# Kernel optimization log

Measured on AMD Instinct MI355X. Metric: run time of the kernel, lower is better.

## Reference

```python
import jax, jax.numpy as jnp
import numpy as np

N_HEAD = 16
LN_EPS = 1e-5


def setup_inputs() -> dict:
    key = jax.random.key(0)
    ks = jax.random.split(key, 12)
    B, S, D = 4, 1024, 1024
    s = 1.0 / np.sqrt(D)
    return {
        "Q": jax.random.normal(ks[0], (B, S, D), jnp.float32),
        "K": jax.random.normal(ks[1], (B, S, D), jnp.float32),
        "V": jax.random.normal(ks[2], (B, S, D), jnp.float32),
        # Linear weights stored torch-style [out, in]
        "Wq": jax.random.normal(ks[3], (D, D), jnp.float32) * s,
        "bq": jnp.zeros((D,), jnp.float32),
        "Wk": jax.random.normal(ks[4], (D, D), jnp.float32) * s,
        "bk": jnp.zeros((D,), jnp.float32),
        "Wv": jax.random.normal(ks[5], (D, D), jnp.float32) * s,
        "bv": jnp.zeros((D,), jnp.float32),
        "Wo": jax.random.normal(ks[6], (D, D), jnp.float32) * s,
        "bo": jnp.zeros((D,), jnp.float32),
        "ln_g": jnp.ones((D,), jnp.float32),
        "ln_b": jnp.zeros((D,), jnp.float32),
    }


def _layer_norm(x, g, b):
    mu = jnp.mean(x, axis=-1, keepdims=True)
    var = jnp.mean(jnp.square(x - mu), axis=-1, keepdims=True)
    return (x - mu) * jax.lax.rsqrt(var + LN_EPS) * g + b


def reference(Q, K, V, Wq, bq, Wk, bk, Wv, bv, Wo, bo, ln_g, ln_b):
    B, S, D = Q.shape
    H = N_HEAD
    dk = D // H
    # projections, split heads: [B, H, S, dk]
    q = (Q @ Wq.T + bq).reshape(B, S, H, dk).transpose(0, 2, 1, 3)
    k = (K @ Wk.T + bk).reshape(B, S, H, dk).transpose(0, 2, 1, 3)
    v = (V @ Wv.T + bv).reshape(B, S, H, dk).transpose(0, 2, 1, 3)
    scores = jnp.einsum("bhqd,bhkd->bhqk", q, k) / np.sqrt(dk)
    # NOTE: original module applies softmax twice (F.softmax then nn.Softmax)
    attn = jax.nn.softmax(jax.nn.softmax(scores, axis=-1), axis=-1)
    ctx = jnp.einsum("bhqk,bhkd->bhqd", attn, v)  # [B, H, S, dk]
    ctx = ctx.transpose(0, 2, 1, 3).reshape(B, S, D)
    out = ctx @ Wo.T + bo
    return _layer_norm(out + Q, ln_g, ln_b)
```

## Files before the change

kernel.cpp:

```cpp
#include <hip/hip_runtime.h>
#include <cstdint>
#include <cstddef>


typedef unsigned short ushort_t;
typedef __attribute__((ext_vector_type(8))) short bf16x8;
typedef __attribute__((ext_vector_type(8))) unsigned short us8;
typedef __attribute__((ext_vector_type(4))) unsigned short us4;
typedef __attribute__((ext_vector_type(4))) float f32x4;

#define MFMA16(a, b, c) __builtin_amdgcn_mfma_f32_16x16x32_bf16((a), (b), (c), 0, 0, 0)

__device__ __forceinline__ float b2f(ushort_t u) {
  union { unsigned int i; float f; } x; x.i = ((unsigned int)u) << 16; return x.f;
}
__device__ __forceinline__ ushort_t f2b(float f) {
  union { unsigned int i; float f; } x; x.f = f;
  unsigned int r = (x.i + 0x7FFFu + ((x.i >> 16) & 1u)) >> 16;
  return (ushort_t)r;
}
__device__ __forceinline__ us8 cvt8(float4 a, float4 b) {
  us8 r;
  r[0] = f2b(a.x); r[1] = f2b(a.y); r[2] = f2b(a.z); r[3] = f2b(a.w);
  r[4] = f2b(b.x); r[5] = f2b(b.y); r[6] = f2b(b.z); r[7] = f2b(b.w);
  return r;
}

__global__ __launch_bounds__(256, 8) void cvt4_kernel(
    const float* __restrict__ w0, const float* __restrict__ w1,
    const float* __restrict__ w2, const float* __restrict__ w3,
    ushort_t* __restrict__ dst) {
  const int which = blockIdx.y;
  const float* src = (which == 0) ? w0 : (which == 1) ? w1 : (which == 2) ? w2 : w3;
  const int i = (blockIdx.x * 256 + threadIdx.x) * 8;
  const float4 a = *(const float4*)(src + i);
  const float4 b = *(const float4*)(src + i + 4);
  *(us8*)(dst + (size_t)which * 1048576 + i) = cvt8(a, b);
}

__global__ __launch_bounds__(256, 6) void qkv_proj_kernel(
    const float* __restrict__ Qin, const float* __restrict__ Kin,
    const float* __restrict__ Vin,
    const ushort_t* __restrict__ wq, const ushort_t* __restrict__ wk,
    const ushort_t* __restrict__ wv,
    const float* __restrict__ bq, const float* __restrict__ bk,
    const float* __restrict__ bv,
    ushort_t* __restrict__ qb, ushort_t* __restrict__ kb,
    ushort_t* __restrict__ vb) {
  __shared__ __align__(16) ushort_t Asl[64 * 32];
  __shared__ __align__(16) ushort_t Bsl[128 * 32];
  const float* A; const ushort_t* W; const float* bias; float scale;
  if (blockIdx.z == 0)      { A = Qin; W = wq; bias = bq; scale = 0.125f; }
  else if (blockIdx.z == 1) { A = Kin; W = wk; bias = bk; scale = 1.0f; }
  else                      { A = Vin; W = wv; bias = bv; scale = 1.0f; }
  const int l = blockIdx.x;
  const int xcd = l & 7, ii = l >> 3;
  const int m0 = (xcd * 8 + (ii >> 3)) * 64;
  const int n0 = (ii & 7) * 128;
  const int tid = threadIdx.x;
  const int wave = tid >> 6, lane = tid & 63;
  const int l15 = lane & 15, quad = lane >> 4;
  const int wn = wave * 32;

  const int ra = tid >> 2, ca = (tid & 3) * 8;
  const int rb1 = (tid + 256) >> 2;

  const float* Ap = A + (size_t)(m0 + ra) * 1024 + ca;
  const ushort_t* Bp0 = W + (size_t)(n0 + ra) * 1024 + ca;
  const ushort_t* Bp1 = W + (size_t)(n0 + rb1) * 1024 + ca;

  float4 al = *(const float4*)(Ap), ah = *(const float4*)(Ap + 4);
  us8 rb0v = *(const us8*)(Bp0);
  us8 rb1v = *(const us8*)(Bp1);

  f32x4 acc[4][2] = {};
  for (int k0 = 0; k0 < 1024; k0 += 32) {
    __syncthreads();
    *(us8*)(Asl + ra * 32 + ca) = cvt8(al, ah);
    *(us8*)(Bsl + ra * 32 + ca) = rb0v;
    *(us8*)(Bsl + rb1 * 32 + ca) = rb1v;
    __syncthreads();
    if (k0 + 32 < 1024) {
      const int k = k0 + 32;
      al = *(const float4*)(Ap + k); ah = *(const float4*)(Ap + k + 4);
      rb0v = *(const us8*)(Bp0 + k);
      rb1v = *(const us8*)(Bp1 + k);
    }
    bf16x8 af[4], bfr[2];
#pragma unroll
    for (int s = 0; s < 4; ++s)
      af[s] = *(const bf16x8*)(Asl + (s * 16 + l15) * 32 + quad * 8);
#pragma unroll
    for (int s = 0; s < 2; ++s)
      bfr[s] = *(const bf16x8*)(Bsl + (wn + s * 16 + l15) * 32 + quad * 8);
#pragma unroll
    for (int ms = 0; ms < 4; ++ms)
#pragma unroll
      for (int ns = 0; ns < 2; ++ns)
        acc[ms][ns] = MFMA16(af[ms], bfr[ns], acc[ms][ns]);
  }

  if (blockIdx.z != 2) {
    ushort_t* outp = (blockIdx.z == 0) ? qb : kb;
#pragma unroll
    for (int ns = 0; ns < 2; ++ns) {
      const int col = n0 + wn + ns * 16 + l15;
      const float bv_ = bias[col];
#pragma unroll
      for (int ms = 0; ms < 4; ++ms) {
        const int rowb = m0 + ms * 16 + quad * 4;
#pragma unroll
        for (int r = 0; r < 4; ++r) {
          outp[(size_t)(rowb + r) * 1024 + col] =
              f2b((acc[ms][ns][r] + bv_) * scale);
        }
      }
    }
  } else {
#pragma unroll
    for (int ns = 0; ns < 2; ++ns) {
      const int col = n0 + wn + ns * 16 + l15;
      const float bv_ = bias[col];
      const int h = col >> 6, d = col & 63;
#pragma unroll
      for (int ms = 0; ms < 4; ++ms) {
        const int i0 = m0 + ms * 16 + quad * 4;
        const int b = i0 >> 10, s0 = i0 & 1023;
        us4 pack;
#pragma unroll
        for (int r = 0; r < 4; ++r) pack[r] = f2b(acc[ms][ns][r] + bv_);
        *(us4*)(vb + ((size_t)(b * 16 + h) * 64 + d) * 1024 + s0) = pack;
      }
    }
  }
}

__global__ __launch_bounds__(256, 4) void attn_kernel(
    const ushort_t* __restrict__ qb, const ushort_t* __restrict__ kb,
    const ushort_t* __restrict__ vb, ushort_t* __restrict__ ctx) {
  __shared__ __align__(16) ushort_t Qs[64 * 72];
  __shared__ __align__(16) ushort_t Ks[64 * 72];
  __shared__ __align__(16) ushort_t Vt[64 * 72];
  __shared__ __align__(16) ushort_t Ps[4][16 * 68];

  const int tid = threadIdx.x, wave = tid >> 6, lane = tid & 63;
  const int l15 = lane & 15, quad = lane >> 4;
  const int l = blockIdx.x;
  const int xcd = l & 7, ii = l >> 3;
  const int bh = xcd * 8 + (ii >> 4);
  const int q0 = (ii & 15) * 64;
  const int b = bh >> 4, h = bh & 15;
  const ushort_t* qg = qb + ((size_t)b << 20) + h * 64;
  const ushort_t* kg = kb + ((size_t)b << 20) + h * 64;
  const ushort_t* vg = vb + ((size_t)bh << 16);

  const int kr0 = tid >> 3, kc0 = (tid & 7) * 8;
  const int kr1 = (tid + 256) >> 3, kc1 = kc0;

  *(us8*)(Qs + kr0 * 72 + kc0) = *(const us8*)(qg + (size_t)(q0 + kr0) * 1024 + kc0);
  *(us8*)(Qs + kr1 * 72 + kc1) = *(const us8*)(qg + (size_t)(q0 + kr1) * 1024 + kc1);

  float z1[4] = {0.f, 0.f, 0.f, 0.f};
  us8 rk0 = *(const us8*)(kg + (size_t)kr0 * 1024 + kc0);
  us8 rk1 = *(const us8*)(kg + (size_t)kr1 * 1024 + kc1);
  for (int kt = 0; kt < 16; ++kt) {
    __syncthreads();
    *(us8*)(Ks + kr0 * 72 + kc0) = rk0;
    *(us8*)(Ks + kr1 * 72 + kc1) = rk1;
    __syncthreads();
    if (kt < 15) {
      rk0 = *(const us8*)(kg + (size_t)((kt + 1) * 64 + kr0) * 1024 + kc0);
      rk1 = *(const us8*)(kg + (size_t)((kt + 1) * 64 + kr1) * 1024 + kc1);
    }
    f32x4 sc[4] = {};
#pragma unroll
    for (int kk = 0; kk < 2; ++kk) {
      const bf16x8 aq = *(const bf16x8*)(Qs + (wave * 16 + l15) * 72 + kk * 32 + quad * 8);
#pragma unroll
      for (int ns = 0; ns < 4; ++ns) {
        const bf16x8 bk_ = *(const bf16x8*)(Ks + (ns * 16 + l15) * 72 + kk * 32 + quad * 8);
        sc[ns] = MFMA16(aq, bk_, sc[ns]);
      }
    }
#pragma unroll
    for (int ns = 0; ns < 4; ++ns)
#pragma unroll
      for (int r = 0; r < 4; ++r) z1[r] += __expf(sc[ns][r]);
  }
  float iz1[4];
#pragma unroll
  for (int r = 0; r < 4; ++r) {
    float s = z1[r];
#pragma unroll
    for (int off = 1; off < 16; off <<= 1) s += __shfl_xor(s, off, 64);
    iz1[r] = 1.0f / s;
  }

  f32x4 oac[4] = {};
  float z2[4] = {0.f, 0.f, 0.f, 0.f};
  rk0 = *(const us8*)(kg + (size_t)kr0 * 1024 + kc0);
  rk1 = *(const us8*)(kg + (size_t)kr1 * 1024 + kc1);
  us8 rv0 = *(const us8*)(vg + (size_t)kr0 * 1024 + kc0);
  us8 rv1 = *(const us8*)(vg + (size_t)kr1 * 1024 + kc1);
  for (int kt = 0; kt < 16; ++kt) {
    __syncthreads();
    *(us8*)(Ks + kr0 * 72 + kc0) = rk0;
    *(us8*)(Ks + kr1 * 72 + kc1) = rk1;
    *(us8*)(Vt + kr0 * 72 + kc0) = rv0;
    *(us8*)(Vt + kr1 * 72 + kc1) = rv1;
    __syncthreads();
    if (kt < 15) {
      rk0 = *(const us8*)(kg + (size_t)((kt + 1) * 64 + kr0) * 1024 + kc0);
      rk1 = *(const us8*)(kg + (size_t)((kt + 1) * 64 + kr1) * 1024 + kc1);
      rv0 = *(const us8*)(vg + (size_t)kr0 * 1024 + (kt + 1) * 64 + kc0);
      rv1 = *(const us8*)(vg + (size_t)kr1 * 1024 + (kt + 1) * 64 + kc1);
    }
    f32x4 sc[4] = {};
#pragma unroll
    for (int kk = 0; kk < 2; ++kk) {
      const bf16x8 aq = *(const bf16x8*)(Qs + (wave * 16 + l15) * 72 + kk * 32 + quad * 8);
#pragma unroll
      for (int ns = 0; ns < 4; ++ns) {
        const bf16x8 bk_ = *(const bf16x8*)(Ks + (ns * 16 + l15) * 72 + kk * 32 + quad * 8);
        sc[ns] = MFMA16(aq, bk_, sc[ns]);
      }
    }
#pragma unroll
    for (int ns = 0; ns < 4; ++ns)
#pragma unroll
      for (int r = 0; r < 4; ++r) {
        const float p1 = __expf(sc[ns][r]) * iz1[r];
        const float e2 = __expf(p1);
        z2[r] += e2;
        Ps[wave][(quad * 4 + r) * 68 + ns * 16 + l15] = f2b(e2);
      }
    __asm__ __volatile__("s_waitcnt lgkmcnt(0)" ::: "memory");
#pragma unroll
    for (int kk = 0; kk < 2; ++kk) {
      const ushort_t* pp = &Ps[wave][l15 * 68 + kk * 32 + quad * 8];
      union { us4 hseg[2]; bf16x8 v; } u;
      u.hseg[0] = *(const us4*)pp;
      u.hseg[1] = *(const us4*)(pp + 4);
      const bf16x8 ap = u.v;
#pragma unroll
      for (int ns2 = 0; ns2 < 4; ++ns2) {
        const bf16x8 bv_ = *(const bf16x8*)(Vt + (ns2 * 16 + l15) * 72 + kk * 32 + quad * 8);
        oac[ns2] = MFMA16(ap, bv_, oac[ns2]);
      }
    }
  }

#pragma unroll
  for (int r = 0; r < 4; ++r) {
    float s = z2[r];
#pragma unroll
    for (int off = 1; off < 16; off <<= 1) s += __shfl_xor(s, off, 64);
    z2[r] = s;
  }
#pragma unroll
  for (int ns2 = 0; ns2 < 4; ++ns2) {
    const int d = ns2 * 16 + l15;
#pragma unroll
    for (int r = 0; r < 4; ++r) {
      const int s = q0 + wave * 16 + quad * 4 + r;
      ctx[((size_t)(b * 1024 + s)) * 1024 + h * 64 + d] = f2b(oac[ns2][r] / z2[r]);
    }
  }
}

__global__ __launch_bounds__(256, 4) void out_proj_kernel(
    const ushort_t* __restrict__ ctxp, const ushort_t* __restrict__ wo,
    const float* __restrict__ bo, ushort_t* __restrict__ pre) {
  __shared__ __align__(16) ushort_t Asl[64 * 32];
  __shared__ __align__(16) ushort_t Bsl[128 * 32];
  const int tid = threadIdx.x;
  const int wave = tid >> 6, lane = tid & 63;
  const int l15 = lane & 15, quad = lane >> 4;
  const int l = blockIdx.x;
  const int xcd = l & 7, ii = l >> 3;
  const int m0 = (xcd * 8 + (ii >> 3)) * 64;
  const int n0 = (ii & 7) * 128;
  const int wn = wave * 32;

  const int ra = tid >> 2, ca = (tid & 3) * 8;
  const int rb1 = (tid + 256) >> 2;

  us8 va = *(const us8*)(ctxp + (size_t)(m0 + ra) * 1024 + ca);
  us8 vb0 = *(const us8*)(wo + (size_t)(n0 + ra) * 1024 + ca);
  us8 vb1 = *(const us8*)(wo + (size_t)(n0 + rb1) * 1024 + ca);

  f32x4 acc[4][2] = {};
  for (int k0 = 0; k0 < 1024; k0 += 32) {
    __syncthreads();
    *(us8*)(Asl + ra * 32 + ca) = va;
    *(us8*)(Bsl + ra * 32 + ca) = vb0;
    *(us8*)(Bsl + rb1 * 32 + ca) = vb1;
    __syncthreads();
    if (k0 + 32 < 1024) {
      const int k = k0 + 32;
      va  = *(const us8*)(ctxp + (size_t)(m0 + ra) * 1024 + k + ca);
      vb0 = *(const us8*)(wo + (size_t)(n0 + ra) * 1024 + k + ca);
      vb1 = *(const us8*)(wo + (size_t)(n0 + rb1) * 1024 + k + ca);
    }
    bf16x8 af[4], bfr[2];
#pragma unroll
    for (int s = 0; s < 4; ++s)
      af[s] = *(const bf16x8*)(Asl + (s * 16 + l15) * 32 + quad * 8);
#pragma unroll
    for (int s = 0; s < 2; ++s)
      bfr[s] = *(const bf16x8*)(Bsl + (wn + s * 16 + l15) * 32 + quad * 8);
#pragma unroll
    for (int ms = 0; ms < 4; ++ms)
#pragma unroll
      for (int ns = 0; ns < 2; ++ns)
        acc[ms][ns] = MFMA16(af[ms], bfr[ns], acc[ms][ns]);
  }

#pragma unroll
  for (int ns = 0; ns < 2; ++ns) {
    const int col = n0 + wn + ns * 16 + l15;
    const float bv_ = bo[col];
#pragma unroll
    for (int ms = 0; ms < 4; ++ms) {
      const int rowb = m0 + ms * 16 + quad * 4;
#pragma unroll
      for (int r = 0; r < 4; ++r) {
        pre[(size_t)(rowb + r) * 1024 + col] = f2b(acc[ms][ns][r] + bv_);
      }
    }
  }
}

__global__ __launch_bounds__(256, 4) void ln_kernel(
    const ushort_t* __restrict__ pre, const float* __restrict__ Q,
    const float* __restrict__ g, const float* __restrict__ bta,
    float* __restrict__ out) {
  const int row = blockIdx.x;
  const int tid = threadIdx.x;
  const size_t base = (size_t)row * 1024 + tid * 4;
  const ushort4 p4 = *(const ushort4*)(pre + base);
  const float4 q4 = *(const float4*)(Q + base);
  float v[4] = {b2f(p4.x) + q4.x, b2f(p4.y) + q4.y,
                b2f(p4.z) + q4.z, b2f(p4.w) + q4.w};
  float s1 = v[0] + v[1] + v[2] + v[3];
  float s2 = v[0]*v[0] + v[1]*v[1] + v[2]*v[2] + v[3]*v[3];
#pragma unroll
  for (int off = 1; off < 64; off <<= 1) {
    s1 += __shfl_xor(s1, off, 64);
    s2 += __shfl_xor(s2, off, 64);
  }
  __shared__ float r1[4], r2[4];
  const int wave = tid >> 6, lane = tid & 63;
  if (lane == 0) { r1[wave] = s1; r2[wave] = s2; }
  __syncthreads();
  const float t1 = r1[0] + r1[1] + r1[2] + r1[3];
  const float t2 = r2[0] + r2[1] + r2[2] + r2[3];
  const float mu = t1 * (1.0f / 1024.0f);
  const float var = t2 * (1.0f / 1024.0f) - mu * mu;
  const float inv = rsqrtf(var + 1e-5f);
  const int c0 = tid * 4;
#pragma unroll
  for (int j = 0; j < 4; ++j) {
    const int c = c0 + j;
    out[(size_t)row * 1024 + c] = (v[j] - mu) * inv * g[c] + bta[c];
  }
}

extern "C" void kernel_launch(void* const* d_in, const int* in_sizes, int n_in,
                              void* d_out, int out_size, void* d_ws, size_t ws_size,
                              hipStream_t stream) {
  const float* Q  = (const float*)d_in[0];
  const float* K  = (const float*)d_in[1];
  const float* V  = (const float*)d_in[2];
  const float* Wq = (const float*)d_in[3];
  const float* bq = (const float*)d_in[4];
  const float* Wk = (const float*)d_in[5];
  const float* bk = (const float*)d_in[6];
  const float* Wv = (const float*)d_in[7];
  const float* bv = (const float*)d_in[8];
  const float* Wo = (const float*)d_in[9];
  const float* bo = (const float*)d_in[10];
  const float* lg = (const float*)d_in[11];
  const float* lb = (const float*)d_in[12];

  char* ws = (char*)d_ws;
  ushort_t* qb  = (ushort_t*)(ws);
  ushort_t* kb  = (ushort_t*)(ws + ((size_t)8  << 20));
  ushort_t* vb  = (ushort_t*)(ws + ((size_t)16 << 20));
  ushort_t* pre = (ushort_t*)(ws);

  ushort_t* dptr  = (ushort_t*)d_out;
  ushort_t* wo_bf = dptr;
  ushort_t* wq_bf = dptr + 1048576;
  ushort_t* wk_bf = dptr + 2097152;
  ushort_t* wv_bf = dptr + 3145728;
  ushort_t* ctx   = dptr + 4194304;
  float*    out   = (float*)d_out;

  cvt4_kernel<<<dim3(512, 4), 256, 0, stream>>>(Wo, Wq, Wk, Wv, dptr);
  qkv_proj_kernel<<<dim3(512, 1, 3), 256, 0, stream>>>(Q, K, V, wq_bf, wk_bf, wv_bf,
                                                       bq, bk, bv, qb, kb, vb);
  attn_kernel<<<dim3(1024), 256, 0, stream>>>(qb, kb, vb, ctx);
  out_proj_kernel<<<dim3(512), 256, 0, stream>>>(ctx, wo_bf, bo, pre);
  ln_kernel<<<dim3(4096), 256, 0, stream>>>(pre, Q, lg, lb, out);
}
```

Baseline: 263.9 us.

## Enlarge projection GEMM tiles to 128x128 and stage bf16 operands via global_load_lds

Both projection GEMMs move from 64x128 to 128x128 block tiles, with waves arranged 2x2 so each wave computes a 64x64 sub-tile. The grid is halved and per-block register and LDS use roughly double. The aim is more operand reuse and MFMA work per LDS fetch. The bf16 weight tiles, and the ctx tiles in out_proj, are now copied straight from global memory into LDS with global_load_lds instead of passing through registers. This drops the register-based prefetch, so out_proj no longer overlaps loads with compute, and with only 256 blocks fewer CUs may be kept busy.

```diff
diff --git a/kernel.cpp b/kernel.cpp
--- a/kernel.cpp
+++ b/kernel.cpp
@@ -24,6 +24,12 @@
   r[0] = f2b(a.x); r[1] = f2b(a.y); r[2] = f2b(a.z); r[3] = f2b(a.w);
   r[4] = f2b(b.x); r[5] = f2b(b.y); r[6] = f2b(b.z); r[7] = f2b(b.w);
   return r;
+}
+
+__device__ __forceinline__ void gll16(const ushort_t* g, ushort_t* l) {
+  __builtin_amdgcn_global_load_lds(
+      (const __attribute__((address_space(1))) void*)g,
+      (__attribute__((address_space(3))) void*)l, 16, 0, 0);
 }
 
 __global__ __launch_bounds__(256, 8) void cvt4_kernel(
@@ -38,7 +44,7 @@
   *(us8*)(dst + (size_t)which * 1048576 + i) = cvt8(a, b);
 }
 
-__global__ __launch_bounds__(256, 6) void qkv_proj_kernel(
+__global__ __launch_bounds__(256, 3) void qkv_proj_kernel(
     const float* __restrict__ Qin, const float* __restrict__ Kin,
     const float* __restrict__ Vin,
     const ushort_t* __restrict__ wq, const ushort_t* __restrict__ wk,
@@ -47,7 +53,7 @@
     const float* __restrict__ bv,
     ushort_t* __restrict__ qb, ushort_t* __restrict__ kb,
     ushort_t* __restrict__ vb) {
-  __shared__ __align__(16) ushort_t Asl[64 * 32];
+  __shared__ __align__(16) ushort_t Asl[128 * 32];
   __shared__ __align__(16) ushort_t Bsl[128 * 32];
   const float* A; const ushort_t* W; const float* bias; float scale;
   if (blockIdx.z == 0)      { A = Qin; W = wq; bias = bq; scale = 0.125f; }
@@ -55,60 +61,61 @@
   else                      { A = Vin; W = wv; bias = bv; scale = 1.0f; }
   const int l = blockIdx.x;
   const int xcd = l & 7, ii = l >> 3;
-  const int m0 = (xcd * 8 + (ii >> 3)) * 64;
+  const int m0 = (xcd * 4 + (ii >> 3)) * 128;
   const int n0 = (ii & 7) * 128;
   const int tid = threadIdx.x;
   const int wave = tid >> 6, lane = tid & 63;
   const int l15 = lane & 15, quad = lane >> 4;
-  const int wn = wave * 32;
+  const int wr = wave >> 1, wc = wave & 1;
 
   const int ra = tid >> 2, ca = (tid & 3) * 8;
-  const int rb1 = (tid + 256) >> 2;
-
-  const float* Ap = A + (size_t)(m0 + ra) * 1024 + ca;
-  const ushort_t* Bp0 = W + (size_t)(n0 + ra) * 1024 + ca;
-  const ushort_t* Bp1 = W + (size_t)(n0 + rb1) * 1024 + ca;
-
-  float4 al = *(const float4*)(Ap), ah = *(const float4*)(Ap + 4);
-  us8 rb0v = *(const us8*)(Bp0);
-  us8 rb1v = *(const us8*)(Bp1);
-
-  f32x4 acc[4][2] = {};
+  const float* Ap0 = A + (size_t)(m0 + ra) * 1024 + ca;
+  const float* Ap1 = A + (size_t)(m0 + ra + 64) * 1024 + ca;
+
+  const int rB0 = wave * 32 + (lane >> 2);
+  const ushort_t* Bg0 = W + (size_t)(n0 + rB0) * 1024 + (lane & 3) * 8;
+  const ushort_t* Bg1 = W + (size_t)(n0 + rB0 + 16) * 1024 + (lane & 3) * 8;
+  ushort_t* Bl0 = Bsl + wave * 1024;
+  ushort_t* Bl1 = Bsl + wave * 1024 + 512;
+
+  float4 a00 = *(const float4*)(Ap0), a01 = *(const float4*)(Ap0 + 4);
+  float4 a10 = *(const float4*)(Ap1), a11 = *(const float4*)(Ap1 + 4);
+
+  f32x4 acc[4][4] = {};
   for (int k0 = 0; k0 < 1024; k0 += 32) {
     __syncthreads();
-    *(us8*)(Asl + ra * 32 + ca) = cvt8(al, ah);
-    *(us8*)(Bsl + ra * 32 + ca) = rb0v;
-    *(us8*)(Bsl + rb1 * 32 + ca) = rb1v;
+    *(us8*)(Asl + ra * 32 + ca) = cvt8(a00, a01);
+    *(us8*)(Asl + (ra + 64) * 32 + ca) = cvt8(a10, a11);
+    gll16(Bg0 + k0, Bl0);
+    gll16(Bg1 + k0, Bl1);
     __syncthreads();
     if (k0 + 32 < 1024) {
-      const int k = k0 + 32;
-      al = *(const float4*)(Ap + k); ah = *(const float4*)(Ap + k + 4);
-      rb0v = *(const us8*)(Bp0 + k);
-      rb1v = *(const us8*)(Bp1 + k);
-    }
-    bf16x8 af[4], bfr[2];
+      a00 = *(const float4*)(Ap0 + k0 + 32); a01 = *(const float4*)(Ap0 + k0 + 36);
+      a10 = *(const float4*)(Ap1 + k0 + 32); a11 = *(const float4*)(Ap1 + k0 + 36);
+    }
+    bf16x8 af[4], bfr[4];
 #pragma unroll
     for (int s = 0; s < 4; ++s)
-      af[s] = *(const bf16x8*)(Asl + (s * 16 + l15) * 32 + quad * 8);
-#pragma unroll
-    for (int s = 0; s < 2; ++s)
-      bfr[s] = *(const bf16x8*)(Bsl + (wn + s * 16 + l15) * 32 + quad * 8);
+      af[s] = *(const bf16x8*)(Asl + (wr * 64 + s * 16 + l15) * 32 + quad * 8);
+#pragma unroll
+    for (int s = 0; s < 4; ++s)
+      bfr[s] = *(const bf16x8*)(Bsl + (wc * 64 + s * 16 + l15) * 32 + quad * 8);
 #pragma unroll
     for (int ms = 0; ms < 4; ++ms)
 #pragma unroll
-      for (int ns = 0; ns < 2; ++ns)
+      for (int ns = 0; ns < 4; ++ns)
         acc[ms][ns] = MFMA16(af[ms], bfr[ns], acc[ms][ns]);
   }
 
   if (blockIdx.z != 2) {
     ushort_t* outp = (blockIdx.z == 0) ? qb : kb;
 #pragma unroll
-    for (int ns = 0; ns < 2; ++ns) {
-      const int col = n0 + wn + ns * 16 + l15;
+    for (int ns = 0; ns < 4; ++ns) {
+      const int col = n0 + wc * 64 + ns * 16 + l15;
       const float bv_ = bias[col];
 #pragma unroll
       for (int ms = 0; ms < 4; ++ms) {
-        const int rowb = m0 + ms * 16 + quad * 4;
+        const int rowb = m0 + wr * 64 + ms * 16 + quad * 4;
 #pragma unroll
         for (int r = 0; r < 4; ++r) {
           outp[(size_t)(rowb + r) * 1024 + col] =
@@ -118,13 +125,13 @@
     }
   } else {
 #pragma unroll
-    for (int ns = 0; ns < 2; ++ns) {
-      const int col = n0 + wn + ns * 16 + l15;
+    for (int ns = 0; ns < 4; ++ns) {
+      const int col = n0 + wc * 64 + ns * 16 + l15;
       const float bv_ = bias[col];
       const int h = col >> 6, d = col & 63;
 #pragma unroll
       for (int ms = 0; ms < 4; ++ms) {
-        const int i0 = m0 + ms * 16 + quad * 4;
+        const int i0 = m0 + wr * 64 + ms * 16 + quad * 4;
         const int b = i0 >> 10, s0 = i0 & 1023;
         us4 pack;
 #pragma unroll
@@ -268,61 +275,60 @@
   }
 }
 
-__global__ __launch_bounds__(256, 4) void out_proj_kernel(
+__global__ __launch_bounds__(256, 3) void out_proj_kernel(
     const ushort_t* __restrict__ ctxp, const ushort_t* __restrict__ wo,
     const float* __restrict__ bo, ushort_t* __restrict__ pre) {
-  __shared__ __align__(16) ushort_t Asl[64 * 32];
+  __shared__ __align__(16) ushort_t Asl[128 * 32];
   __shared__ __align__(16) ushort_t Bsl[128 * 32];
   const int tid = threadIdx.x;
   const int wave = tid >> 6, lane = tid & 63;
   const int l15 = lane & 15, quad = lane >> 4;
+  const int wr = wave >> 1, wc = wave & 1;
   const int l = blockIdx.x;
   const int xcd = l & 7, ii = l >> 3;
-  const int m0 = (xcd * 8 + (ii >> 3)) * 64;
+  const int m0 = (xcd * 4 + (ii >> 3)) * 128;
   const int n0 = (ii & 7) * 128;
-  const int wn = wave * 32;
-
-  const int ra = tid >> 2, ca = (tid & 3) * 8;
-  const int rb1 = (tid + 256) >> 2;
-
-  us8 va = *(const us8*)(ctxp + (size_t)(m0 + ra) * 1024 + ca);
-  us8 vb0 = *(const us8*)(wo + (size_t)(n0 + ra) * 1024 + ca);
-  us8 vb1 = *(const us8*)(wo + (size_t)(n0 + rb1) * 1024 + ca);
-
-  f32x4 acc[4][2] = {};
+
+  const int rr = wave * 32 + (lane >> 2);
+  const int cc = (lane & 3) * 8;
+  const ushort_t* Ag0 = ctxp + (size_t)(m0 + rr) * 1024 + cc;
+  const ushort_t* Ag1 = ctxp + (size_t)(m0 + rr + 16) * 1024 + cc;
+  const ushort_t* Bg0 = wo + (size_t)(n0 + rr) * 1024 + cc;
+  const ushort_t* Bg1 = wo + (size_t)(n0 + rr + 16) * 1024 + cc;
+  ushort_t* Al0 = Asl + wave * 1024;
+  ushort_t* Al1 = Asl + wave * 1024 + 512;
+  ushort_t* Bl0 = Bsl + wave * 1024;
+  ushort_t* Bl1 = Bsl + wave * 1024 + 512;
+
+  f32x4 acc[4][4] = {};
   for (int k0 = 0; k0 < 1024; k0 += 32) {
     __syncthreads();
-    *(us8*)(Asl + ra * 32 + ca) = va;
-    *(us8*)(Bsl + ra * 32 + ca) = vb0;
-    *(us8*)(Bsl + rb1 * 32 + ca) = vb1;
-    __syncthreads();
-    if (k0 + 32 < 1024) {
-      const int k = k0 + 32;
-      va  = *(const us8*)(ctxp + (size_t)(m0 + ra) * 1024 + k + ca);
-      vb0 = *(const us8*)(wo + (size_t)(n0 + ra) * 1024 + k + ca);
-      vb1 = *(const us8*)(wo + (size_t)(n0 + rb1) * 1024 + k + ca);
-    }
-    bf16x8 af[4], bfr[2];
+    gll16(Ag0 + k0, Al0);
+    gll16(Ag1 + k0, Al1);
+    gll16(Bg0 + k0, Bl0);
+    gll16(Bg1 + k0, Bl1);
+    __syncthreads();
+    bf16x8 af[4], bfr[4];
 #pragma unroll
     for (int s = 0; s < 4; ++s)
-      af[s] = *(const bf16x8*)(Asl + (s * 16 + l15) * 32 + quad * 8);
-#pragma unroll
-    for (int s = 0; s < 2; ++s)
-      bfr[s] = *(const bf16x8*)(Bsl + (wn + s * 16 + l15) * 32 + quad * 8);
+      af[s] = *(const bf16x8*)(Asl + (wr * 64 + s * 16 + l15) * 32 + quad * 8);
+#pragma unroll
+    for (int s = 0; s < 4; ++s)
+      bfr[s] = *(const bf16x8*)(Bsl + (wc * 64 + s * 16 + l15) * 32 + quad * 8);
 #pragma unroll
     for (int ms = 0; ms < 4; ++ms)
 #pragma unroll
-      for (int ns = 0; ns < 2; ++ns)
+      for (int ns = 0; ns < 4; ++ns)
         acc[ms][ns] = MFMA16(af[ms], bfr[ns], acc[ms][ns]);
   }
 
 #pragma unroll
-  for (int ns = 0; ns < 2; ++ns) {
-    const int col = n0 + wn + ns * 16 + l15;
+  for (int ns = 0; ns < 4; ++ns) {
+    const int col = n0 + wc * 64 + ns * 16 + l15;
     const float bv_ = bo[col];
 #pragma unroll
     for (int ms = 0; ms < 4; ++ms) {
-      const int rowb = m0 + ms * 16 + quad * 4;
+      const int rowb = m0 + wr * 64 + ms * 16 + quad * 4;
 #pragma unroll
       for (int r = 0; r < 4; ++r) {
         pre[(size_t)(rowb + r) * 1024 + col] = f2b(acc[ms][ns][r] + bv_);
@@ -398,9 +404,9 @@
   float*    out   = (float*)d_out;
 
   cvt4_kernel<<<dim3(512, 4), 256, 0, stream>>>(Wo, Wq, Wk, Wv, dptr);
-  qkv_proj_kernel<<<dim3(512, 1, 3), 256, 0, stream>>>(Q, K, V, wq_bf, wk_bf, wv_bf,
+  qkv_proj_kernel<<<dim3(256, 1, 3), 256, 0, stream>>>(Q, K, V, wq_bf, wk_bf, wv_bf,
                                                        bq, bk, bv, qb, kb, vb);
   attn_kernel<<<dim3(1024), 256, 0, stream>>>(qb, kb, vb, ctx);
-  out_proj_kernel<<<dim3(512), 256, 0, stream>>>(ctx, wo_bf, bo, pre);
+  out_proj_kernel<<<dim3(256), 256, 0, stream>>>(ctx, wo_bf, bo, pre);
   ln_kernel<<<dim3(4096), 256, 0, stream>>>(pre, Q, lg, lb, out);
 }
```

Result: faster. 247.0 us (-6.4%).
